# Performance work log

Hardware: AMD Instinct MI355X
Metric: run time of the kernel (lower is better)

Reference implementation:

```python
import jax, jax.numpy as jnp
import numpy as np

B, T, D = 8, 1024, 1024
KD, VD, H = 1024, 1024, 16  # key_dim_total, value_dim_total, num_heads
NEG = -1e9
EPS = 1e-5


def setup_inputs() -> dict:
    key = jax.random.key(0)
    ks = jax.random.split(key, 8)
    x = jax.random.normal(ks[0], (B, T, D), dtype=jnp.float32)
    x_lens = jax.random.randint(ks[1], (B,), 1, T + 1).astype(jnp.int32)
    ln_gamma = jnp.ones((D,), jnp.float32)
    ln_beta = jnp.zeros((D,), jnp.float32)
    qkv_out = 2 * KD + VD
    w_qkv = jax.random.normal(ks[2], (D, qkv_out), jnp.float32) / np.sqrt(D)
    b_qkv = jax.random.normal(ks[3], (qkv_out,), jnp.float32) * 0.01
    w_out = jax.random.normal(ks[4], (VD, D), jnp.float32) / np.sqrt(VD)
    b_out = jax.random.normal(ks[5], (D,), jnp.float32) * 0.01
    return {"x": x, "x_lens": x_lens, "ln_gamma": ln_gamma, "ln_beta": ln_beta,
            "w_qkv": w_qkv, "b_qkv": b_qkv, "w_out": w_out, "b_out": b_out}


def reference(x, x_lens, ln_gamma, ln_beta, w_qkv, b_qkv, w_out, b_out):
    # LayerNorm over feature dim
    mu = jnp.mean(x, axis=-1, keepdims=True)
    var = jnp.mean(jnp.square(x - mu), axis=-1, keepdims=True)
    xn = (x - mu) * jax.lax.rsqrt(var + EPS) * ln_gamma + ln_beta
    # fused QKV projection
    qkv = xn @ w_qkv + b_qkv  # (B, T, 2*KD+VD)
    q, k, v = qkv[..., :KD], qkv[..., KD:2 * KD], qkv[..., 2 * KD:]
    hd = KD // H
    q = q.reshape(B, T, H, hd).transpose(0, 2, 1, 3)  # (B,H,T,hd)
    k = k.reshape(B, T, H, hd).transpose(0, 2, 1, 3)
    v = v.reshape(B, T, H, VD // H).transpose(0, 2, 1, 3)
    scale = 1.0 / np.sqrt(hd)
    scores = jnp.einsum("bhtd,bhsd->bhts", q, k) * scale  # (B,H,T,T)
    # combined causal + kv-length padding mask (additive in original; boolean here)
    causal = jnp.tril(jnp.ones((T, T), bool))  # (T,T)
    kv_valid = jnp.arange(T)[None, :] < x_lens[:, None]  # (B,T)
    mask = causal[None, None, :, :] & kv_valid[:, None, None, :]
    scores = jnp.where(mask, scores, NEG)
    att = jax.nn.softmax(scores, axis=-1)
    att_out = jnp.einsum("bhts,bhsd->bhtd", att, v)  # (B,H,T,hd_v)
    out = att_out.transpose(0, 2, 1, 3).reshape(B, T, VD)
    out = out @ w_out + b_out
    return out
```

## Files before the change

kernel.cpp:

```cpp
#include <hip/hip_runtime.h>

#define D_MODEL 1024
#define T_SEQ   1024
#define BATCH   8
#define NHEAD   16
#define HDIM    64

typedef float      v4f   __attribute__((ext_vector_type(4)));
typedef _Float16   half8 __attribute__((ext_vector_type(8)));
typedef _Float16   half4h __attribute__((ext_vector_type(4)));
typedef unsigned int ui4 __attribute__((ext_vector_type(4)));

__device__ __forceinline__ void load_lds16(const _Float16* g, _Float16* l) {
  __builtin_amdgcn_global_load_lds(
      (const __attribute__((address_space(1))) unsigned int*)g,
      (__attribute__((address_space(3))) unsigned int*)l, 16, 0, 0);
}

__global__ __launch_bounds__(256) void ln_kernel(const float* __restrict__ x,
                                                 const float* __restrict__ gamma,
                                                 const float* __restrict__ beta,
                                                 _Float16* __restrict__ xn) {
  int row = blockIdx.x;
  int tid = threadIdx.x;
  const float* xr = x + (size_t)row * D_MODEL;
  v4f xv = *(const v4f*)(xr + tid * 4);
  float s  = xv[0] + xv[1] + xv[2] + xv[3];
  float sq = xv[0]*xv[0] + xv[1]*xv[1] + xv[2]*xv[2] + xv[3]*xv[3];
#pragma unroll
  for (int off = 32; off > 0; off >>= 1) {
    s  += __shfl_xor(s, off);
    sq += __shfl_xor(sq, off);
  }
  __shared__ float ps[4], psq[4];
  int wave = tid >> 6;
  if ((tid & 63) == 0) { ps[wave] = s; psq[wave] = sq; }
  __syncthreads();
  float tot  = ps[0] + ps[1] + ps[2] + ps[3];
  float totq = psq[0] + psq[1] + psq[2] + psq[3];
  float mean = tot * (1.0f / D_MODEL);
  float var  = totq * (1.0f / D_MODEL) - mean * mean;
  float rs   = rsqrtf(var + 1e-5f);
  v4f gv = *(const v4f*)(gamma + tid * 4);
  v4f bv = *(const v4f*)(beta + tid * 4);
  half4h o;
#pragma unroll
  for (int i = 0; i < 4; ++i)
    o[i] = (_Float16)((xv[i] - mean) * rs * gv[i] + bv[i]);
  *(half4h*)(xn + (size_t)row * D_MODEL + tid * 4) = o;
}

__global__ __launch_bounds__(256) void fragize_kernel(const float* __restrict__ W,
                                                      _Float16* __restrict__ Bf,
                                                      int N, int K) {
  int g = blockIdx.x * 256 + threadIdx.x;
  int lane = g & 63, tile = g >> 6;
  int ktiles = K >> 5;
  int kt = tile % ktiles, nt = tile / ktiles;
  int n  = nt * 16 + (lane & 15);
  int k0 = kt * 32 + (lane >> 4) * 8;
  half8 o;
#pragma unroll
  for (int j = 0; j < 8; ++j) o[j] = (_Float16)W[(size_t)(k0 + j) * N + n];
  *(half8*)(Bf + (size_t)g * 8) = o;
}

__global__ __launch_bounds__(256) void wtrans_kernel(const float* __restrict__ W,
                                                     _Float16* __restrict__ Wt,
                                                     int N, int K) {
  __shared__ _Float16 t[64][72];
  int k0 = blockIdx.x * 64, n0 = blockIdx.y * 64;
  int tid = threadIdx.x;
  int r = tid >> 3, c = (tid & 7) * 8;
#pragma unroll
  for (int it = 0; it < 2; ++it) {
    int row = r + it * 32;
    const float* src = W + (size_t)(k0 + row) * N + n0 + c;
    v4f x0 = *(const v4f*)src;
    v4f x1 = *(const v4f*)(src + 4);
#pragma unroll
    for (int j = 0; j < 4; ++j) t[row][c + j] = (_Float16)x0[j];
#pragma unroll
    for (int j = 0; j < 4; ++j) t[row][c + 4 + j] = (_Float16)x1[j];
  }
  __syncthreads();
#pragma unroll
  for (int it = 0; it < 2; ++it) {
    int d = r + it * 32;
    half8 o;
#pragma unroll
    for (int j = 0; j < 8; ++j) o[j] = t[c + j][d];
    *(half8*)(Wt + (size_t)(n0 + d) * K + k0 + c) = o;
  }
}

__global__ __launch_bounds__(256) void vtrans_kernel(const _Float16* __restrict__ Vd,
                                                     _Float16* __restrict__ Vt) {
  __shared__ _Float16 tile[64][68];
  int p  = blockIdx.y;
  int t0 = blockIdx.x * 64;
  int tid = threadIdx.x;
  int r = tid >> 3, c = (tid & 7) * 8;
#pragma unroll
  for (int it = 0; it < 2; ++it) {
    int rr = r + it * 32;
    *(ui4*)&tile[rr][c] = *(const ui4*)&Vd[((size_t)p * T_SEQ + t0 + rr) * HDIM + c];
  }
  __syncthreads();
#pragma unroll
  for (int it = 0; it < 2; ++it) {
    int d = r + it * 32;
    half8 o;
#pragma unroll
    for (int j = 0; j < 8; ++j) o[j] = tile[c + j][d];
    *(half8*)&Vt[((size_t)p * HDIM + d) * T_SEQ + t0 + c] = o;
  }
}


#define BAR   __builtin_amdgcn_s_barrier()
#define LGKM0 asm volatile("s_waitcnt lgkmcnt(0)" ::: "memory")
#define VMC2  asm volatile("s_waitcnt vmcnt(2)" ::: "memory")
#define PRIO1 __builtin_amdgcn_s_setprio(1)
#define PRIO0 __builtin_amdgcn_s_setprio(0)

#define RDA(dst, BUF, MI0, KK)                                                  \
  _Pragma("unroll")                                                             \
  for (int d2 = 0; d2 < 4; ++d2)                                                \
    dst[d2] = *(const half8*)(lds + (BUF) +                                     \
                              (wm + ((MI0) + d2) * 16 + l15) * 64 +             \
                              ((((KK) * 4 + quad) ^ swz) * 8));

#define RDB(dst, BUF, KK)                                                       \
  _Pragma("unroll")                                                             \
  for (int ni = 0; ni < 4; ++ni)                                                \
    dst[ni] = *(const half8*)(lds + (BUF) + 16384 +                             \
                              (wn + ni * 16 + l15) * 64 +                       \
                              ((((KK) * 4 + quad) ^ swz) * 8));

#define MFQ(MI0, A_, B_)                                                        \
  _Pragma("unroll")                                                             \
  for (int mi = 0; mi < 4; ++mi)                                                \
    _Pragma("unroll")                                                           \
    for (int ni = 0; ni < 4; ++ni)                                              \
      acc[(MI0) + mi][ni] = __builtin_amdgcn_mfma_f32_16x16x32_f16(             \
          A_[mi], B_[ni], acc[(MI0) + mi][ni], 0, 0, 0);

#define STGA(BUF, R0, KT)                                                       \
  load_lds16(Asrc + (size_t)(R0) * 1024 + (KT) * 64, ldst + (BUF) + (R0) * 64)
#define STGB(BUF, R0, KT)                                                       \
  load_lds16(Bsrc + (size_t)(R0) * 1024 + (KT) * 64, ldst + (BUF) + 16384 + (R0) * 64)
#define HTA(BUF, HH, KT) { STGA(BUF, (HH)*128, KT); STGA(BUF, (HH)*128 + 64, KT); }
#define HTB(BUF, KT)     { STGB(BUF, 0, KT);   STGB(BUF, 64, KT);                 \
                           STGB(BUF, 128, KT); STGB(BUF, 192, KT); }

__global__ __launch_bounds__(512, 2) void gemm256_qkv(
    const _Float16* __restrict__ A, const _Float16* __restrict__ Bt,
    const float* __restrict__ bias,
    _Float16* __restrict__ Qd, _Float16* __restrict__ Kd, _Float16* __restrict__ Vd) {
  __shared__ _Float16 lds[65536];
  const int K = 1024;
  int tid  = threadIdx.x;
  int wave = tid >> 6, lane = tid & 63;
  int l15  = lane & 15, quad = lane >> 4;
  int wm = (wave & 1) * 128, wn = (wave >> 1) * 64;
  int m0 = blockIdx.x * 256, n0 = blockIdx.y * 256;
  int swz = l15 & 7;

  int ric = tid >> 3;
  int colofs = ((tid & 7) ^ (ric & 7)) * 8;
  const _Float16* Asrc = A  + (size_t)(m0 + ric) * K + colofs;
  const _Float16* Bsrc = Bt + (size_t)(n0 + ric) * K + colofs;
  _Float16* ldst = lds + wave * 512;

  const int B0 = 0, B1 = 32768;
  v4f acc[8][4];
  v4f zero = {0.f, 0.f, 0.f, 0.f};
#pragma unroll
  for (int i = 0; i < 8; ++i)
#pragma unroll
    for (int j = 0; j < 4; ++j) acc[i][j] = zero;

  HTA(B0, 0, 0); HTA(B0, 1, 0); HTB(B0, 0);
  HTA(B1, 0, 1);
  VMC2; BAR;

  half8 a0[4], a1[4], b0[4], b1[4];
#pragma unroll 1
  for (int i = 0; i < 8; ++i) {
    int kt1 = 2 * i + 1;
    int kt2 = (2 * i + 2 < 16) ? 2 * i + 2 : 15;
    int kt3 = (2 * i + 3 < 16) ? 2 * i + 3 : 15;
    RDA(a0, B0, 0, 0); RDB(b0, B0, 0);
    HTA(B1, 1, kt1);
    BAR; LGKM0; PRIO1; MFQ(0, a0, b0); PRIO0; BAR;
    RDA(a1, B0, 4, 0);
    HTB(B1, kt1);
    BAR; LGKM0; PRIO1; MFQ(4, a1, b0); PRIO0; BAR;
    RDA(a0, B0, 0, 1); RDA(a1, B0, 4, 1); RDB(b1, B0, 1);
    BAR; LGKM0; PRIO1; MFQ(0, a0, b1); PRIO0; BAR;
    HTA(B0, 0, kt2);
    VMC2; BAR; PRIO1; MFQ(4, a1, b1); PRIO0; BAR;
    RDA(a0, B1, 0, 0); RDB(b0, B1, 0);
    HTA(B0, 1, kt2);
    BAR; LGKM0; PRIO1; MFQ(0, a0, b0); PRIO0; BAR;
    RDA(a1, B1, 4, 0);
    HTB(B0, kt2);
    BAR; LGKM0; PRIO1; MFQ(4, a1, b0); PRIO0; BAR;
    RDA(a0, B1, 0, 1); RDA(a1, B1, 4, 1); RDB(b1, B1, 1);
    BAR; LGKM0; PRIO1; MFQ(0, a0, b1); PRIO0; BAR;
    HTA(B1, 0, kt3);
    VMC2; BAR; PRIO1; MFQ(4, a1, b1); PRIO0; BAR;
  }

  float bv[4];
#pragma unroll
  for (int ni = 0; ni < 4; ++ni) bv[ni] = bias[n0 + wn + ni * 16 + l15];
  int sec = n0 >> 10;
  _Float16* dstP = sec == 0 ? Qd : (sec == 1 ? Kd : Vd);
  float scale = sec == 0 ? 0.18033688f : 1.0f;
#pragma unroll
  for (int mi = 0; mi < 8; ++mi)
#pragma unroll
    for (int ni = 0; ni < 4; ++ni) {
      int n = n0 + wn + ni * 16 + l15;
      int h = (n >> 6) & 15, d = n & 63;
#pragma unroll
      for (int r = 0; r < 4; ++r) {
        int m = m0 + wm + mi * 16 + quad * 4 + r;
        int b = m >> 10, t = m & 1023;
        float v = acc[mi][ni][r] + bv[ni];
        dstP[((size_t)(b * NHEAD + h) * T_SEQ + t) * HDIM + d] = (_Float16)(v * scale);
      }
    }
}

template <int MODE>
__global__ __launch_bounds__(256) void gemm_kernel(
    const _Float16* __restrict__ A, const _Float16* __restrict__ Bfrag,
    const float* __restrict__ bias, int M, int N, int K,
    float* __restrict__ outF,
    _Float16* __restrict__ Qd, _Float16* __restrict__ Kd, _Float16* __restrict__ Vd) {
  __shared__ _Float16 As[2][128 * 32];
  int tid = threadIdx.x;
  int wave = tid >> 6, lane = tid & 63;
  int l15 = lane & 15, quad = lane >> 4;
  int wm = (wave & 1) * 64, wn = (wave >> 1) * 64;
  int m0 = blockIdx.x * 128, n0 = blockIdx.y * 128;
  v4f zero = {0.f, 0.f, 0.f, 0.f};
  v4f acc[4][4];
#pragma unroll
  for (int i = 0; i < 4; ++i)
#pragma unroll
    for (int j = 0; j < 4; ++j) acc[i][j] = zero;

  int ar0 = tid >> 2;
  int akc = (tid & 3) * 8;
  const _Float16* Ap = A + (size_t)(m0 + ar0) * K + akc;
  _Float16* AsW0 = &As[0][0] + wave * 512;
  _Float16* AsW1 = &As[1][0] + wave * 512;
  const int ktiles = K >> 5;
  const _Float16* Bp = Bfrag + (size_t)((n0 + wn) >> 4) * ktiles * 512 + lane * 8;

  load_lds16(Ap, AsW0);
  load_lds16(Ap + (size_t)64 * K, AsW0 + 2048);
  for (int kt = 0; kt < ktiles; ++kt) {
    int cur = kt & 1;
    __syncthreads();
    if (kt + 1 < ktiles) {
      _Float16* nx = cur ? AsW0 : AsW1;
      load_lds16(Ap + (kt + 1) * 32,                  nx);
      load_lds16(Ap + (kt + 1) * 32 + (size_t)64 * K, nx + 2048);
    }
    half8 bf[4];
#pragma unroll
    for (int ni = 0; ni < 4; ++ni)
      bf[ni] = *(const half8*)(Bp + ((size_t)ni * ktiles + kt) * 512);
    half8 af[4];
#pragma unroll
    for (int i = 0; i < 4; ++i)
      af[i] = *(const half8*)&As[cur][(wm + i * 16 + l15) * 32 + quad * 8];
#pragma unroll
    for (int mi = 0; mi < 4; ++mi)
#pragma unroll
      for (int ni = 0; ni < 4; ++ni)
        acc[mi][ni] = __builtin_amdgcn_mfma_f32_16x16x32_f16(af[mi], bf[ni], acc[mi][ni], 0, 0, 0);
  }
  float bv[4];
#pragma unroll
  for (int ni = 0; ni < 4; ++ni) bv[ni] = bias[n0 + wn + ni * 16 + l15];
#pragma unroll
  for (int mi = 0; mi < 4; ++mi) {
#pragma unroll
    for (int ni = 0; ni < 4; ++ni) {
      int n = n0 + wn + ni * 16 + l15;
#pragma unroll
      for (int r = 0; r < 4; ++r) {
        int m = m0 + wm + mi * 16 + quad * 4 + r;
        float v = acc[mi][ni][r] + bv[ni];
        if (MODE == 1) {
          outF[(size_t)m * N + n] = v;
        } else {
          int b = m >> 10, t = m & 1023;
          int h = (n >> 6) & 15, d = n & 63;
          size_t idx = ((size_t)(b * NHEAD + h) * T_SEQ + t) * HDIM + d;
          if (n < 1024)        Qd[idx] = (_Float16)(v * 0.18033688f);
          else if (n < 2048)   Kd[idx] = (_Float16)v;
          else                 Vd[idx] = (_Float16)v;
        }
      }
    }
  }
}

__global__ __launch_bounds__(256) void attn_kernel(const _Float16* __restrict__ Qg,
                                                   const _Float16* __restrict__ Kk,
                                                   const _Float16* __restrict__ Vt,
                                                   const int* __restrict__ x_lens,
                                                   _Float16* __restrict__ att) {
  __shared__ _Float16 Ks[2][64 * 32];
  __shared__ _Float16 Vs[2][64 * 32];
  __shared__ _Float16 Pb[4][16 * 72];
  int blk = blockIdx.x;
  int qt = blk >> 7;
  int bh = blk & 127;
  int h  = bh & 15;
  int b  = bh >> 4;
  int t0 = qt * 64;
  int len = x_lens[b];
  int tid = threadIdx.x;
  int wave = tid >> 6, lane = tid & 63;
  int l15 = lane & 15, quad = lane >> 4;
  size_t plane = (size_t)(b * NHEAD + h) * (T_SEQ * HDIM);
  int qrow = t0 + wave * 16;
  int qabs = qrow + l15;
  const _Float16* Qp = Qg + plane + (size_t)qabs * HDIM + quad * 8;
  half8 qf0 = *(const half8*)Qp;
  half8 qf1 = *(const half8*)(Qp + 32);
  v4f zero = {0.f, 0.f, 0.f, 0.f};
  float m_i = -1e30f, l_i = 0.f;
  v4f Ov[4];
#pragma unroll
  for (int nt = 0; nt < 4; ++nt) Ov[nt] = zero;

  int jmaxb = min(t0 + 63, len - 1);
  int ntile = (jmaxb >> 6) + 1;
  int wjmax = min(qrow + 15, len - 1);

  const _Float16* src[4];
  _Float16* dst[4];
  int strd[4];
#pragma unroll
  for (int i = 0; i < 4; ++i) {
    int u = wave * 4 + i;
    int q = u & 3, hf = (u >> 2) & 1;
    if (u < 8) {
      src[i] = Kk + plane + (size_t)(q * 16 + (lane >> 2)) * HDIM + hf * 32 + (lane & 3) * 8;
      dst[i] = &Ks[hf][0] + q * 512;
      strd[i] = 64 * HDIM;
    } else {
      src[i] = Vt + plane + (size_t)(q * 16 + (lane >> 2)) * T_SEQ + hf * 32 + (lane & 3) * 8;
      dst[i] = &Vs[hf][0] + q * 512;
      strd[i] = 64;
    }
  }

  for (int jt = 0; jt < ntile; ++jt) {
    int j0 = jt * 64;
    __syncthreads();
#pragma unroll
    for (int i = 0; i < 4; ++i) {
      load_lds16(src[i], dst[i]);
      src[i] += strd[i];
    }
    __syncthreads();
    if (j0 <= wjmax) {
      v4f s[4];
#pragma unroll
      for (int nt = 0; nt < 4; ++nt) {
        s[nt] = zero;
        half8 k0 = *(const half8*)&Ks[0][(nt * 16 + l15) * 32 + quad * 8];
        half8 k1 = *(const half8*)&Ks[1][(nt * 16 + l15) * 32 + quad * 8];
        s[nt] = __builtin_amdgcn_mfma_f32_16x16x32_f16(k0, qf0, s[nt], 0, 0, 0);
        s[nt] = __builtin_amdgcn_mfma_f32_16x16x32_f16(k1, qf1, s[nt], 0, 0, 0);
      }
      float mnew = m_i;
      bool full = (j0 + 63 <= qrow) && (j0 + 63 < len);
      if (full) {
#pragma unroll
        for (int nt = 0; nt < 4; ++nt)
#pragma unroll
          for (int r = 0; r < 4; ++r)
            mnew = fmaxf(mnew, s[nt][r]);
      } else {
#pragma unroll
        for (int nt = 0; nt < 4; ++nt) {
#pragma unroll
          for (int r = 0; r < 4; ++r) {
            int key = j0 + nt * 16 + quad * 4 + r;
            float v = (key <= qabs && key < len) ? s[nt][r] : -1e30f;
            s[nt][r] = v;
            mnew = fmaxf(mnew, v);
          }
        }
      }
      mnew = fmaxf(mnew, __shfl_xor(mnew, 16));
      mnew = fmaxf(mnew, __shfl_xor(mnew, 32));
      float alpha = exp2f(m_i - mnew);
      m_i = mnew;
      float rsum = 0.f;
#pragma unroll
      for (int nt = 0; nt < 4; ++nt)
#pragma unroll
        for (int r = 0; r < 4; ++r) {
          float p = exp2f(s[nt][r] - mnew);
          s[nt][r] = p;
          rsum += p;
        }
      rsum += __shfl_xor(rsum, 16);
      rsum += __shfl_xor(rsum, 32);
      l_i = l_i * alpha + rsum;
#pragma unroll
      for (int nt = 0; nt < 4; ++nt)
#pragma unroll
        for (int r = 0; r < 4; ++r) Ov[nt][r] *= alpha;
#pragma unroll
      for (int nt = 0; nt < 4; ++nt) {
        half4h pk;
#pragma unroll
        for (int r = 0; r < 4; ++r) pk[r] = (_Float16)s[nt][r];
        *(half4h*)&Pb[wave][l15 * 72 + nt * 16 + quad * 4] = pk;
      }
      asm volatile("s_waitcnt lgkmcnt(0)" ::: "memory");
      half8 pf0 = *(const half8*)&Pb[wave][l15 * 72 + quad * 8];
      half8 pf1 = *(const half8*)&Pb[wave][l15 * 72 + 32 + quad * 8];
#pragma unroll
      for (int nt = 0; nt < 4; ++nt) {
        half8 v0 = *(const half8*)&Vs[0][(nt * 16 + l15) * 32 + quad * 8];
        half8 v1 = *(const half8*)&Vs[1][(nt * 16 + l15) * 32 + quad * 8];
        Ov[nt] = __builtin_amdgcn_mfma_f32_16x16x32_f16(v0, pf0, Ov[nt], 0, 0, 0);
        Ov[nt] = __builtin_amdgcn_mfma_f32_16x16x32_f16(v1, pf1, Ov[nt], 0, 0, 0);
      }
    }
  }
  float inv = 1.0f / l_i;
#pragma unroll
  for (int nt = 0; nt < 4; ++nt) {
    half4h ok;
#pragma unroll
    for (int r = 0; r < 4; ++r) ok[r] = (_Float16)(Ov[nt][r] * inv);
    *(half4h*)&Pb[wave][l15 * 72 + nt * 16 + quad * 4] = ok;
  }
  asm volatile("s_waitcnt lgkmcnt(0)" ::: "memory");
  int r0 = lane >> 3, c0 = (lane & 7) * 8;
  half8 o0 = *(const half8*)&Pb[wave][r0 * 72 + c0];
  half8 o1 = *(const half8*)&Pb[wave][(r0 + 8) * 72 + c0];
  *(half8*)&att[((size_t)(b * T_SEQ) + qrow + r0) * D_MODEL + h * HDIM + c0] = o0;
  *(half8*)&att[((size_t)(b * T_SEQ) + qrow + r0 + 8) * D_MODEL + h * HDIM + c0] = o1;
}

extern "C" void kernel_launch(void* const* d_in, const int* in_sizes, int n_in,
                              void* d_out, int out_size, void* d_ws, size_t ws_size,
                              hipStream_t stream) {
  const float* x        = (const float*)d_in[0];
  const int*   x_lens   = (const int*)d_in[1];
  const float* ln_gamma = (const float*)d_in[2];
  const float* ln_beta  = (const float*)d_in[3];
  const float* w_qkv    = (const float*)d_in[4];
  const float* b_qkv    = (const float*)d_in[5];
  const float* w_out    = (const float*)d_in[6];
  const float* b_out    = (const float*)d_in[7];
  float* out = (float*)d_out;

  char* w = (char*)d_ws;
  _Float16* xn    = (_Float16*)w; w += (size_t)8192 * 1024 * 2;
  _Float16* WtQKV = (_Float16*)w; w += (size_t)3072 * 1024 * 2;
  _Float16* BfOut = (_Float16*)w; w += (size_t)1024 * 1024 * 2;
  _Float16* Qd    = (_Float16*)w; w += (size_t)8192 * 1024 * 2;
  _Float16* Kd    = (_Float16*)w; w += (size_t)8192 * 1024 * 2;
  _Float16* Vd    = (_Float16*)w; w += (size_t)8192 * 1024 * 2;
  _Float16* att   = (_Float16*)w; w += (size_t)8192 * 1024 * 2;
  _Float16* Vt    = xn;

  wtrans_kernel<<<dim3(16, 48), 256, 0, stream>>>(w_qkv, WtQKV, 3072, 1024);
  fragize_kernel<<<(1024 * 1024 / 8) / 256, 256, 0, stream>>>(w_out, BfOut, 1024, 1024);
  ln_kernel<<<8192, 256, 0, stream>>>(x, ln_gamma, ln_beta, xn);
  gemm256_qkv<<<dim3(32, 12), 512, 0, stream>>>(xn, WtQKV, b_qkv, Qd, Kd, Vd);
  vtrans_kernel<<<dim3(16, 128), 256, 0, stream>>>(Vd, Vt);
  attn_kernel<<<2048, 256, 0, stream>>>(Qd, Kd, Vt, x_lens, att);
  gemm_kernel<1><<<dim3(8192 / 128, 1024 / 128), 256, 0, stream>>>(
      att, BfOut, b_out, 8192, 1024, 1024, out, nullptr, nullptr, nullptr);
}
```

Baseline: 254.7 us.

## Restructure QKV GEMM mainloop into 4-stage K=32 LDS pipeline

The QKV GEMM main loop is rewritten from a double-buffered K=64 scheme with many barriers to a four-buffer ring of K=32 tiles. Each tile is loaded three tiles ahead, and each step needs only one barrier and a counted vmcnt wait. The LDS layout also changes from an XOR-swizzled row layout to a pair-interleaved layout with new read offsets. The aim is to cut barrier and waitcnt stalls and keep more global loads in flight. The cost is more per-iteration overhead from smaller K steps and a possible change in LDS bank conflicts.

```diff
diff --git a/kernel.cpp b/kernel.cpp
--- a/kernel.cpp
+++ b/kernel.cpp
@@ -119,61 +119,70 @@
 
 
 #define BAR   __builtin_amdgcn_s_barrier()
-#define LGKM0 asm volatile("s_waitcnt lgkmcnt(0)" ::: "memory")
-#define VMC2  asm volatile("s_waitcnt vmcnt(2)" ::: "memory")
 #define PRIO1 __builtin_amdgcn_s_setprio(1)
 #define PRIO0 __builtin_amdgcn_s_setprio(0)
 
-#define RDA(dst, BUF, MI0, KK)                                                  \
-  _Pragma("unroll")                                                             \
-  for (int d2 = 0; d2 < 4; ++d2)                                                \
-    dst[d2] = *(const half8*)(lds + (BUF) +                                     \
-                              (wm + ((MI0) + d2) * 16 + l15) * 64 +             \
-                              ((((KK) * 4 + quad) ^ swz) * 8));
-
-#define RDB(dst, BUF, KK)                                                       \
-  _Pragma("unroll")                                                             \
-  for (int ni = 0; ni < 4; ++ni)                                                \
-    dst[ni] = *(const half8*)(lds + (BUF) + 16384 +                             \
-                              (wn + ni * 16 + l15) * 64 +                       \
-                              ((((KK) * 4 + quad) ^ swz) * 8));
-
-#define MFQ(MI0, A_, B_)                                                        \
-  _Pragma("unroll")                                                             \
-  for (int mi = 0; mi < 4; ++mi)                                                \
-    _Pragma("unroll")                                                           \
-    for (int ni = 0; ni < 4; ++ni)                                              \
-      acc[(MI0) + mi][ni] = __builtin_amdgcn_mfma_f32_16x16x32_f16(             \
-          A_[mi], B_[ni], acc[(MI0) + mi][ni], 0, 0, 0);
-
-#define STGA(BUF, R0, KT)                                                       \
-  load_lds16(Asrc + (size_t)(R0) * 1024 + (KT) * 64, ldst + (BUF) + (R0) * 64)
-#define STGB(BUF, R0, KT)                                                       \
-  load_lds16(Bsrc + (size_t)(R0) * 1024 + (KT) * 64, ldst + (BUF) + 16384 + (R0) * 64)
-#define HTA(BUF, HH, KT) { STGA(BUF, (HH)*128, KT); STGA(BUF, (HH)*128 + 64, KT); }
-#define HTB(BUF, KT)     { STGB(BUF, 0, KT);   STGB(BUF, 64, KT);                 \
-                           STGB(BUF, 128, KT); STGB(BUF, 192, KT); }
+#define STG4(BUFH2, KT)                                                          \
+  {                                                                              \
+    load_lds16(Asrc + (KT) * 32,              lds + (BUFH2) + wave * 512);       \
+    load_lds16(Asrc + 128 * 1024 + (KT) * 32, lds + (BUFH2) + 4096 + wave * 512);\
+    load_lds16(Bsrc + (KT) * 32,              lds + (BUFH2) + 8192 + wave * 512);\
+    load_lds16(Bsrc + 128 * 1024 + (KT) * 32, lds + (BUFH2) + 12288 + wave * 512);\
+  }
+
+#define TILE(T, BUFH, VN, DS)                                                    \
+  {                                                                              \
+    BAR;                                                                         \
+    __builtin_amdgcn_sched_barrier(0);                                           \
+    asm volatile("s_waitcnt vmcnt(" #VN ")" ::: "memory");                       \
+    half8 a[8], b[4];                                                            \
+    _Pragma("unroll")                                                            \
+    for (int mi = 0; mi < 4; ++mi)                                               \
+      a[mi] = *(const half8*)(lds + (BUFH) + rdA + mi * 512);                    \
+    _Pragma("unroll")                                                            \
+    for (int ni = 0; ni < 4; ++ni)                                               \
+      b[ni] = *(const half8*)(lds + (BUFH) + rdB + ni * 512);                    \
+    if (DS) STG4((((T) + 3) & 3) * 16384, (T) + 3);                              \
+    _Pragma("unroll")                                                            \
+    for (int mi = 4; mi < 8; ++mi)                                               \
+      a[mi] = *(const half8*)(lds + (BUFH) + rdA + mi * 512);                    \
+    PRIO1;                                                                       \
+    _Pragma("unroll")                                                            \
+    for (int mi = 0; mi < 4; ++mi)                                               \
+      _Pragma("unroll")                                                          \
+      for (int ni = 0; ni < 4; ++ni)                                             \
+        acc[mi][ni] = __builtin_amdgcn_mfma_f32_16x16x32_f16(a[mi], b[ni],       \
+                                                             acc[mi][ni], 0,0,0);\
+    _Pragma("unroll")                                                            \
+    for (int mi = 4; mi < 8; ++mi)                                               \
+      _Pragma("unroll")                                                          \
+      for (int ni = 0; ni < 4; ++ni)                                             \
+        acc[mi][ni] = __builtin_amdgcn_mfma_f32_16x16x32_f16(a[mi], b[ni],       \
+                                                             acc[mi][ni], 0,0,0);\
+    PRIO0;                                                                       \
+  }
 
 __global__ __launch_bounds__(512, 2) void gemm256_qkv(
     const _Float16* __restrict__ A, const _Float16* __restrict__ Bt,
     const float* __restrict__ bias,
     _Float16* __restrict__ Qd, _Float16* __restrict__ Kd, _Float16* __restrict__ Vd) {
   __shared__ _Float16 lds[65536];
-  const int K = 1024;
   int tid  = threadIdx.x;
   int wave = tid >> 6, lane = tid & 63;
   int l15  = lane & 15, quad = lane >> 4;
   int wm = (wave & 1) * 128, wn = (wave >> 1) * 64;
   int m0 = blockIdx.x * 256, n0 = blockIdx.y * 256;
-  int swz = l15 & 7;
-
-  int ric = tid >> 3;
-  int colofs = ((tid & 7) ^ (ric & 7)) * 8;
-  const _Float16* Asrc = A  + (size_t)(m0 + ric) * K + colofs;
-  const _Float16* Bsrc = Bt + (size_t)(n0 + ric) * K + colofs;
-  _Float16* ldst = lds + wave * 512;
-
-  const int B0 = 0, B1 = 32768;
+
+  int arow = 2 * (tid >> 3) + ((tid >> 2) & 1);
+  int akch = tid & 3;
+  const _Float16* Asrc = A  + (size_t)(m0 + arow) * 1024 + akch * 8;
+  const _Float16* Bsrc = Bt + (size_t)(n0 + arow) * 1024 + akch * 8;
+
+  int p8  = l15 >> 1;
+  int c8r = (l15 & 1) * 4 + quad;
+  int rdA = wm * 32 + p8 * 64 + c8r * 8;
+  int rdB = 8192 + wn * 32 + p8 * 64 + c8r * 8;
+
   v4f acc[8][4];
   v4f zero = {0.f, 0.f, 0.f, 0.f};
 #pragma unroll
@@ -181,37 +190,19 @@
 #pragma unroll
     for (int j = 0; j < 4; ++j) acc[i][j] = zero;
 
-  HTA(B0, 0, 0); HTA(B0, 1, 0); HTB(B0, 0);
-  HTA(B1, 0, 1);
-  VMC2; BAR;
-
-  half8 a0[4], a1[4], b0[4], b1[4];
+  STG4(0, 0); STG4(16384, 1); STG4(32768, 2);
+
 #pragma unroll 1
-  for (int i = 0; i < 8; ++i) {
-    int kt1 = 2 * i + 1;
-    int kt2 = (2 * i + 2 < 16) ? 2 * i + 2 : 15;
-    int kt3 = (2 * i + 3 < 16) ? 2 * i + 3 : 15;
-    RDA(a0, B0, 0, 0); RDB(b0, B0, 0);
-    HTA(B1, 1, kt1);
-    BAR; LGKM0; PRIO1; MFQ(0, a0, b0); PRIO0; BAR;
-    RDA(a1, B0, 4, 0);
-    HTB(B1, kt1);
-    BAR; LGKM0; PRIO1; MFQ(4, a1, b0); PRIO0; BAR;
-    RDA(a0, B0, 0, 1); RDA(a1, B0, 4, 1); RDB(b1, B0, 1);
-    BAR; LGKM0; PRIO1; MFQ(0, a0, b1); PRIO0; BAR;
-    HTA(B0, 0, kt2);
-    VMC2; BAR; PRIO1; MFQ(4, a1, b1); PRIO0; BAR;
-    RDA(a0, B1, 0, 0); RDB(b0, B1, 0);
-    HTA(B0, 1, kt2);
-    BAR; LGKM0; PRIO1; MFQ(0, a0, b0); PRIO0; BAR;
-    RDA(a1, B1, 4, 0);
-    HTB(B0, kt2);
-    BAR; LGKM0; PRIO1; MFQ(4, a1, b0); PRIO0; BAR;
-    RDA(a0, B1, 0, 1); RDA(a1, B1, 4, 1); RDB(b1, B1, 1);
-    BAR; LGKM0; PRIO1; MFQ(0, a0, b1); PRIO0; BAR;
-    HTA(B1, 0, kt3);
-    VMC2; BAR; PRIO1; MFQ(4, a1, b1); PRIO0; BAR;
-  }
+  for (int tt = 0; tt < 28; tt += 4) {
+    TILE(tt + 0, 0,     8, 1);
+    TILE(tt + 1, 16384, 8, 1);
+    TILE(tt + 2, 32768, 8, 1);
+    TILE(tt + 3, 49152, 8, 1);
+  }
+  TILE(28, 0,     8, 1);
+  TILE(29, 16384, 8, 0);
+  TILE(30, 32768, 4, 0);
+  TILE(31, 49152, 0, 0);
 
   float bv[4];
 #pragma unroll
```

After: 266.2 us. 4.5% more time.
